# Kernel tuning notes

Hardware: AMD Instinct MI355X
Metric: run time of the kernel (lower is better)

The kernel has to match this reference:

```python
import jax, jax.numpy as jnp
import numpy as np

N_NODES = 20000
N_EDGES = 5000
STEPS = 50
INFECTION_RATE = 0.01
RECOVERY_RATE = 0.038
EDGE_DENSITY = 0.002  # ~10 hyperedges per node on average


def setup_inputs() -> dict:
    key = jax.random.key(0)
    k1, k2 = jax.random.split(key, 2)
    # initial SIR state per node: valid probability rows summing to 1
    u = jax.random.uniform(k1, (N_NODES, 3), dtype=jnp.float32)
    x = u / u.sum(axis=1, keepdims=True)
    # binary hypergraph incidence matrix (num_hyperedges, num_nodes)
    H = (jax.random.uniform(k2, (N_EDGES, N_NODES)) < EDGE_DENSITY).astype(jnp.float32)
    beta = jnp.full((N_NODES,), INFECTION_RATE, dtype=jnp.float32)
    gamma = jnp.full((N_NODES,), RECOVERY_RATE, dtype=jnp.float32)
    return {"x": x, "H": H, "beta": beta, "gamma": gamma, "steps": STEPS}


def reference(x, H, beta, gamma, steps):
    # x: (N, 3) [S, I, R] per node; H: (E, N) incidence.
    def step(state, _):
        S, I, R = state[:, 0], state[:, 1], state[:, 2]
        # hypergraph message passing: node -> hyperedge -> node
        new_cases = beta * (S * (H.T @ (H @ I)))
        new_recovery = gamma * I
        nxt = jnp.stack(
            [S - new_cases, I + new_cases - new_recovery, R + new_recovery], axis=1
        )
        nxt = jnp.maximum(nxt, 0.0)                       # clamp(min=0)
        nxt = nxt / nxt.sum(axis=1, keepdims=True)        # per-node row normalize
        return nxt, nxt

    _, traj = jax.lax.scan(step, x, None, length=steps - 1)
    # output[0] = initial state, then steps-1 simulated updates -> (steps, N, 3)
    return jnp.concatenate([x[None], traj], axis=0)
```

## Files before the change

kernel.cpp:

```cpp
#include <hip/hip_runtime.h>


#define EDGE_CAP 96
#define NODE_CAP 32
#define NIDX_REG 16
#define COOP_BLOCKS 256
#define COOP_THREADS 512
#define BAR_UINTS 512
#define GRP_STRIDE 16
#define NGRP 16

__global__ void zero_counts_kernel(int* edge_cnt, int* node_cnt, unsigned* bar,
                                   int n_edges, int n_nodes) {
    int i = blockIdx.x * blockDim.x + threadIdx.x;
    if (i < BAR_UINTS) bar[i] = 0u;
    if (i < n_edges) edge_cnt[i] = 0;
    if (i < n_nodes) node_cnt[i] = 0;
}

__global__ void build_adjacency_kernel(const float* __restrict__ H,
                                       int* __restrict__ edge_cnt,
                                       int* __restrict__ edge_nodes,
                                       int* __restrict__ node_cnt,
                                       int* __restrict__ node_edges,
                                       int n_nodes) {
    __shared__ int cnt;
    __shared__ int cols[EDGE_CAP];
    const int e = blockIdx.x;
    if (threadIdx.x == 0) cnt = 0;
    __syncthreads();
    const uint4* row4 = (const uint4*)(H + (size_t)e * n_nodes);
    const int n4 = n_nodes >> 2;
    for (int c4 = threadIdx.x; c4 < n4; c4 += blockDim.x) {
        uint4 v = row4[c4];
        if ((v.x | v.y | v.z | v.w) != 0u) {
            int cbase = c4 << 2;
            if (v.x) { int p = atomicAdd(&cnt, 1); if (p < EDGE_CAP) cols[p] = cbase; }
            if (v.y) { int p = atomicAdd(&cnt, 1); if (p < EDGE_CAP) cols[p] = cbase + 1; }
            if (v.z) { int p = atomicAdd(&cnt, 1); if (p < EDGE_CAP) cols[p] = cbase + 2; }
            if (v.w) { int p = atomicAdd(&cnt, 1); if (p < EDGE_CAP) cols[p] = cbase + 3; }
        }
    }
    if (threadIdx.x == 0) {
        const float* row = H + (size_t)e * n_nodes;
        for (int c = n4 << 2; c < n_nodes; ++c)
            if (row[c] != 0.0f) { int p = atomicAdd(&cnt, 1); if (p < EDGE_CAP) cols[p] = c; }
    }
    __syncthreads();
    int cn = min(cnt, EDGE_CAP);
    if (threadIdx.x == 0) edge_cnt[e] = cn;
    for (int i = threadIdx.x; i < cn; i += blockDim.x) {
        int c = cols[i];
        edge_nodes[e * EDGE_CAP + i] = c;
        int q = atomicAdd(&node_cnt[c], 1);
        if (q < NODE_CAP) node_edges[c * NODE_CAP + q] = e;
    }
}

__device__ __forceinline__ float coh_load(const float* p) {
    return __hip_atomic_load(p, __ATOMIC_RELAXED, __HIP_MEMORY_SCOPE_AGENT);
}
__device__ __forceinline__ void coh_storef(float* p, float v) {
    __hip_atomic_store(p, v, __ATOMIC_RELAXED, __HIP_MEMORY_SCOPE_AGENT);
}

__device__ __forceinline__ void bar_arrive(unsigned* bar) {
    asm volatile("s_waitcnt vmcnt(0)" ::: "memory");
    __syncthreads();
    if (threadIdx.x == 0)
        __hip_atomic_fetch_add(&bar[(blockIdx.x >> 4) * GRP_STRIDE], 1u,
                               __ATOMIC_RELAXED, __HIP_MEMORY_SCOPE_AGENT);
}
__device__ __forceinline__ void bar_wait(unsigned* bar, unsigned phase) {
    if (threadIdx.x == 0) {
        unsigned* root = &bar[NGRP * GRP_STRIDE];
        if ((blockIdx.x & 15) == 0) {
            unsigned* grp = &bar[(blockIdx.x >> 4) * GRP_STRIDE];
            while (__hip_atomic_load(grp, __ATOMIC_RELAXED, __HIP_MEMORY_SCOPE_AGENT) < 16u * phase)
                __builtin_amdgcn_s_sleep(1);
            __hip_atomic_fetch_add(root, 1u, __ATOMIC_RELAXED, __HIP_MEMORY_SCOPE_AGENT);
        }
        while (__hip_atomic_load(root, __ATOMIC_RELAXED, __HIP_MEMORY_SCOPE_AGENT) < (unsigned)NGRP * phase)
            __builtin_amdgcn_s_sleep(1);
    }
    __syncthreads();
    asm volatile("" ::: "memory");
}

__global__ __launch_bounds__(COOP_THREADS) void sir_steps_kernel(
        const float* __restrict__ x,
        const int* __restrict__ edge_cnt, const int* __restrict__ edge_nodes,
        const int* __restrict__ node_cnt, const int* __restrict__ node_edges,
        const float* __restrict__ beta, const float* __restrict__ gamma,
        float* __restrict__ y, float* __restrict__ I,
        float* __restrict__ out,
        int n_nodes, int n_edges, int steps, unsigned* bar) {
    const int b  = blockIdx.x;
    const int tx = threadIdx.x;

    const int node_chunk = (n_nodes + gridDim.x - 1) / gridDim.x;
    const int edge_chunk = (n_edges + gridDim.x - 1) / gridDim.x;
    const int wave = tx >> 6, lane = tx & 63;
    const int lslot = wave + (lane << 3);
    const int n = b * node_chunk + lslot;
    const bool own = (lslot < node_chunk) && (n < n_nodes);

    const int k = tx >> 4, gl = tx & 15;
    const int lg = (k & 3) * 8 + (k >> 2);
    const int e = b * edge_chunk + lg;
    const bool has_edge = (lg < edge_chunk) && (e < n_edges);

    int ecnt = 0;
    const int* en = edge_nodes;
    if (has_edge) { ecnt = min(edge_cnt[e], EDGE_CAP); en = edge_nodes + e * EDGE_CAP; }
    int eidx[6];
    #pragma unroll
    for (int i = 0; i < 6; ++i) {
        int j = i * 16 + gl;
        eidx[i] = (has_edge && j < ecnt) ? en[j] : n_nodes;
    }

    int ncnt = 0;
    const int* ne = node_edges;
    float bet = 0.0f, gam = 0.0f;
    if (own) { ncnt = min(node_cnt[n], NODE_CAP); ne = node_edges + n * NODE_CAP;
               bet = beta[n]; gam = gamma[n]; }
    int nidx[NIDX_REG];
    #pragma unroll
    for (int i = 0; i < NIDX_REG; ++i)
        nidx[i] = (own && i < ncnt) ? ne[i] : n_edges;

    float s = 0.0f, iv = 0.0f, r = 0.0f;
    if (own) {
        s = x[n * 3 + 0]; iv = x[n * 3 + 1]; r = x[n * 3 + 2];
        coh_storef(&I[n], iv);
        out[n * 3 + 0] = s; out[n * 3 + 1] = iv; out[n * 3 + 2] = r;
    }
    if (b == 0 && tx == 0) { coh_storef(&I[n_nodes], 0.0f); coh_storef(&y[n_edges], 0.0f); }
    unsigned phase = 1;
    bar_arrive(bar); bar_wait(bar, phase);

    for (int t = 1; t < steps; ++t) {
        if (has_edge) {
            float a0 = coh_load(&I[eidx[0]]);
            float a1 = coh_load(&I[eidx[1]]);
            float a2 = coh_load(&I[eidx[2]]);
            float a3 = coh_load(&I[eidx[3]]);
            float a4 = coh_load(&I[eidx[4]]);
            float a5 = coh_load(&I[eidx[5]]);
            float acc = a0 + a1 + a2 + a3 + a4 + a5;
            acc += __shfl_down(acc, 8, 16);
            acc += __shfl_down(acc, 4, 16);
            acc += __shfl_down(acc, 2, 16);
            acc += __shfl_down(acc, 1, 16);
            if (gl == 0) coh_storef(&y[e], acc);
        }
        ++phase; bar_arrive(bar); bar_wait(bar, phase);

        if (own) {
            float tv[NIDX_REG];
            #pragma unroll
            for (int i = 0; i < NIDX_REG; ++i) tv[i] = coh_load(&y[nidx[i]]);
            float z = 0.0f;
            #pragma unroll
            for (int i = 0; i < NIDX_REG; ++i) z += tv[i];
            for (int i = NIDX_REG; i < ncnt; ++i) z += coh_load(&y[ne[i]]);
            float nc = bet * s * z;
            float nr = gam * iv;
            float s2 = fmaxf(s - nc, 0.0f);
            float i2 = fmaxf(iv + nc - nr, 0.0f);
            float r2 = fmaxf(r + nr, 0.0f);
            float inv = 1.0f / (s2 + i2 + r2);
            s = s2 * inv; iv = i2 * inv; r = r2 * inv;
            coh_storef(&I[n], iv);
        }
        ++phase; bar_arrive(bar);
        if (own) {
            float* ot = out + (size_t)t * n_nodes * 3 + (size_t)n * 3;
            ot[0] = s; ot[1] = iv; ot[2] = r;
        }
        if (t + 1 < steps) bar_wait(bar, phase);
    }
}

extern "C" void kernel_launch(void* const* d_in, const int* in_sizes, int n_in,
                              void* d_out, int out_size, void* d_ws, size_t ws_size,
                              hipStream_t stream) {
    const float* x     = (const float*)d_in[0];
    const float* H     = (const float*)d_in[1];
    const float* beta  = (const float*)d_in[2];
    const float* gamma = (const float*)d_in[3];
    float* out = (float*)d_out;

    const int n_nodes = in_sizes[0] / 3;
    const int n_edges = in_sizes[1] / n_nodes;
    const int steps   = out_size / in_sizes[0];

    char* ws = (char*)d_ws;
    unsigned* bar     = (unsigned*)ws;                    ws += BAR_UINTS * 4;
    int*   edge_cnt   = (int*)ws;                         ws += (size_t)n_edges * 4;
    int*   node_cnt   = (int*)ws;                         ws += (size_t)n_nodes * 4;
    int*   edge_nodes = (int*)ws;                         ws += (size_t)n_edges * EDGE_CAP * 4;
    int*   node_edges = (int*)ws;                         ws += (size_t)n_nodes * NODE_CAP * 4;
    float* y          = (float*)ws;                       ws += ((size_t)n_edges + 1) * 4;
    float* I          = (float*)ws;                       ws += ((size_t)n_nodes + 1) * 4;

    {
        int mx = max(n_edges, max(n_nodes, BAR_UINTS));
        zero_counts_kernel<<<(mx + 255) / 256, 256, 0, stream>>>(edge_cnt, node_cnt, bar,
                                                                 n_edges, n_nodes);
    }
    build_adjacency_kernel<<<n_edges, 256, 0, stream>>>(H, edge_cnt, edge_nodes,
                                                        node_cnt, node_edges, n_nodes);
    sir_steps_kernel<<<COOP_BLOCKS, COOP_THREADS, 0, stream>>>(
        x, edge_cnt, edge_nodes, node_cnt, node_edges, beta, gamma,
        y, I, out, n_nodes, n_edges, steps, bar);
}
```

Measured before the change: 1.088 ms.

## Replace hierarchical grid barrier with flat striped counters and contiguous thread mapping

Replaces the two-level tree grid barrier (group counters plus a root counter) with eight counters on separate cache lines. Each block increments one counter and every waiter polls and sums all eight against a cumulative target. This removes the serial group-leader hop from the critical path of each of the roughly hundred barriers per run, but every block now issues eight loads per poll. It also switches node and edge ownership from an interleaved wave/lane mapping to a contiguous per-thread mapping, which changes coalescing of the state and output accesses.

```diff
diff --git a/kernel.cpp b/kernel.cpp
--- a/kernel.cpp
+++ b/kernel.cpp
@@ -6,9 +6,9 @@
 #define NIDX_REG 16
 #define COOP_BLOCKS 256
 #define COOP_THREADS 512
-#define BAR_UINTS 512
-#define GRP_STRIDE 16
-#define NGRP 16
+#define BAR_LINES 8
+#define BAR_STRIDE 128
+#define BAR_UINTS (BAR_LINES * BAR_STRIDE)
 
 __global__ void zero_counts_kernel(int* edge_cnt, int* node_cnt, unsigned* bar,
                                    int n_edges, int n_nodes) {
@@ -68,20 +68,20 @@
     asm volatile("s_waitcnt vmcnt(0)" ::: "memory");
     __syncthreads();
     if (threadIdx.x == 0)
-        __hip_atomic_fetch_add(&bar[(blockIdx.x >> 4) * GRP_STRIDE], 1u,
+        __hip_atomic_fetch_add(&bar[(blockIdx.x & (BAR_LINES - 1)) * BAR_STRIDE], 1u,
                                __ATOMIC_RELAXED, __HIP_MEMORY_SCOPE_AGENT);
 }
-__device__ __forceinline__ void bar_wait(unsigned* bar, unsigned phase) {
+__device__ __forceinline__ void bar_wait(unsigned* bar, unsigned target) {
     if (threadIdx.x == 0) {
-        unsigned* root = &bar[NGRP * GRP_STRIDE];
-        if ((blockIdx.x & 15) == 0) {
-            unsigned* grp = &bar[(blockIdx.x >> 4) * GRP_STRIDE];
-            while (__hip_atomic_load(grp, __ATOMIC_RELAXED, __HIP_MEMORY_SCOPE_AGENT) < 16u * phase)
-                __builtin_amdgcn_s_sleep(1);
-            __hip_atomic_fetch_add(root, 1u, __ATOMIC_RELAXED, __HIP_MEMORY_SCOPE_AGENT);
-        }
-        while (__hip_atomic_load(root, __ATOMIC_RELAXED, __HIP_MEMORY_SCOPE_AGENT) < (unsigned)NGRP * phase)
+        for (;;) {
+            unsigned sum = 0;
+            #pragma unroll
+            for (int i = 0; i < BAR_LINES; ++i)
+                sum += __hip_atomic_load(&bar[i * BAR_STRIDE], __ATOMIC_RELAXED,
+                                         __HIP_MEMORY_SCOPE_AGENT);
+            if (sum >= target) break;
             __builtin_amdgcn_s_sleep(1);
+        }
     }
     __syncthreads();
     asm volatile("" ::: "memory");
@@ -100,15 +100,12 @@
 
     const int node_chunk = (n_nodes + gridDim.x - 1) / gridDim.x;
     const int edge_chunk = (n_edges + gridDim.x - 1) / gridDim.x;
-    const int wave = tx >> 6, lane = tx & 63;
-    const int lslot = wave + (lane << 3);
-    const int n = b * node_chunk + lslot;
-    const bool own = (lslot < node_chunk) && (n < n_nodes);
+    const int n = b * node_chunk + tx;
+    const bool own = (tx < node_chunk) && (n < n_nodes);
 
     const int k = tx >> 4, gl = tx & 15;
-    const int lg = (k & 3) * 8 + (k >> 2);
-    const int e = b * edge_chunk + lg;
-    const bool has_edge = (lg < edge_chunk) && (e < n_edges);
+    const int e = b * edge_chunk + k;
+    const bool has_edge = (k < edge_chunk) && (e < n_edges);
 
     int ecnt = 0;
     const int* en = edge_nodes;
@@ -137,8 +134,8 @@
         out[n * 3 + 0] = s; out[n * 3 + 1] = iv; out[n * 3 + 2] = r;
     }
     if (b == 0 && tx == 0) { coh_storef(&I[n_nodes], 0.0f); coh_storef(&y[n_edges], 0.0f); }
-    unsigned phase = 1;
-    bar_arrive(bar); bar_wait(bar, phase);
+    unsigned bars = 0;
+    bar_arrive(bar); bars += gridDim.x; bar_wait(bar, bars);
 
     for (int t = 1; t < steps; ++t) {
         if (has_edge) {
@@ -155,7 +152,7 @@
             acc += __shfl_down(acc, 1, 16);
             if (gl == 0) coh_storef(&y[e], acc);
         }
-        ++phase; bar_arrive(bar); bar_wait(bar, phase);
+        bar_arrive(bar); bars += gridDim.x; bar_wait(bar, bars);
 
         if (own) {
             float tv[NIDX_REG];
@@ -174,12 +171,12 @@
             s = s2 * inv; iv = i2 * inv; r = r2 * inv;
             coh_storef(&I[n], iv);
         }
-        ++phase; bar_arrive(bar);
+        bar_arrive(bar); bars += gridDim.x;
         if (own) {
             float* ot = out + (size_t)t * n_nodes * 3 + (size_t)n * 3;
             ot[0] = s; ot[1] = iv; ot[2] = r;
         }
-        if (t + 1 < steps) bar_wait(bar, phase);
+        if (t + 1 < steps) bar_wait(bar, bars);
     }
 }
 
@@ -197,7 +194,7 @@
     const int steps   = out_size / in_sizes[0];
 
     char* ws = (char*)d_ws;
-    unsigned* bar     = (unsigned*)ws;                    ws += BAR_UINTS * 4;
+    unsigned* bar     = (unsigned*)ws;                    ws += (size_t)BAR_UINTS * 4;
     int*   edge_cnt   = (int*)ws;                         ws += (size_t)n_edges * 4;
     int*   node_cnt   = (int*)ws;                         ws += (size_t)n_nodes * 4;
     int*   edge_nodes = (int*)ws;                         ws += (size_t)n_edges * EDGE_CAP * 4;
@@ -206,7 +203,7 @@
     float* I          = (float*)ws;                       ws += ((size_t)n_nodes + 1) * 4;
 
     {
-        int mx = max(n_edges, max(n_nodes, BAR_UINTS));
+        int mx = max(n_edges, max(n_nodes, (int)BAR_UINTS));
         zero_counts_kernel<<<(mx + 255) / 256, 256, 0, stream>>>(edge_cnt, node_cnt, bar,
                                                                  n_edges, n_nodes);
     }
```

Result: faster. 1.011 ms (-7.0%).
